# Kernel optimization log

Measured on AMD Instinct MI355X. Metric: run time of the kernel, lower is better.

Reference implementation:

```python
import jax, jax.numpy as jnp
import numpy as np

NUM_CLASSES = 7
EPS = 1e-10
BATCH = 4_000_000


def setup_inputs() -> dict:
    key = jax.random.key(0)
    k1, k2 = jax.random.split(key)
    logits = jax.random.normal(k1, (BATCH, NUM_CLASSES), dtype=jnp.float32)
    targets = jax.random.randint(k2, (BATCH,), 0, NUM_CLASSES, dtype=jnp.int32)
    return {"logits": logits, "targets": targets}


def reference(logits, targets):
    # softmax probabilities [B, C]
    probs = jax.nn.softmax(logits, axis=1)
    B = logits.shape[0]
    rows = jnp.arange(B)
    t = targets.astype(jnp.int32)
    # sum of probs at classes t-1, t, t+1, masking out-of-range neighbors
    total = probs[rows, t]
    lo = t - 1
    hi = t + 1
    total = total + jnp.where(lo >= 0, probs[rows, jnp.maximum(lo, 0)], 0.0)
    total = total + jnp.where(hi < NUM_CLASSES, probs[rows, jnp.minimum(hi, NUM_CLASSES - 1)], 0.0)
    loss = -jnp.log(total + EPS)
    return jnp.sum(loss) / B
```

## Files before the change

kernel.cpp:

```cpp
#include <hip/hip_runtime.h>
#include <hip/hip_bf16.h>

#define NUM_CLASSES 7
#define ROWS_PER_TILE 256
#define BLOCK 256
#define NBLOCKS 2048
#define F4_PER_TILE (ROWS_PER_TILE * NUM_CLASSES / 4)

__global__ __launch_bounds__(BLOCK) void pom_main(const float* __restrict__ logits,
                                                  const int* __restrict__ targets,
                                                  double* __restrict__ partials,
                                                  int B) {
    __shared__ float4 tile4[F4_PER_TILE];
    float* tile = (float*)tile4;

    const int tid = threadIdx.x;
    const int numTiles = (B + ROWS_PER_TILE - 1) / ROWS_PER_TILE;
    const float4* __restrict__ g4 = (const float4*)logits;
    const long long totalF4 = ((long long)B * NUM_CLASSES) / 4;

    float acc = 0.0f;

    for (int t = blockIdx.x; t < numTiles; t += gridDim.x) {
        const long long f4base = (long long)t * F4_PER_TILE;
        const int row = t * ROWS_PER_TILE + tid;

        int tg = 0;
        if (row < B) tg = targets[row];
        float4 a = make_float4(0.f, 0.f, 0.f, 0.f);
        float4 b = make_float4(0.f, 0.f, 0.f, 0.f);
        if (f4base + tid < totalF4)        a = g4[f4base + tid];
        if (tid < F4_PER_TILE - BLOCK && f4base + BLOCK + tid < totalF4)
                                           b = g4[f4base + BLOCK + tid];

        __syncthreads();
        tile4[tid] = a;
        if (tid < F4_PER_TILE - BLOCK) tile4[BLOCK + tid] = b;
        __syncthreads();

        if (row < B) {
            const float* l = tile + tid * NUM_CLASSES;
            float lv[7];
            #pragma unroll
            for (int i = 0; i < NUM_CLASSES; ++i) lv[i] = l[i];

            float m = lv[0];
            #pragma unroll
            for (int i = 1; i < NUM_CLASSES; ++i) m = fmaxf(m, lv[i]);

            float s = 0.0f, w = 0.0f;
            #pragma unroll
            for (int i = 0; i < NUM_CLASSES; ++i) {
                float e = __expf(lv[i] - m);
                s += e;
                bool in = (i >= tg - 1) && (i <= tg + 1);
                w += in ? e : 0.0f;
            }
            float total = w / s;
            acc += -__logf(total + 1e-10f);
        }
    }

    double d = (double)acc;
    #pragma unroll
    for (int off = 32; off > 0; off >>= 1) d += __shfl_down(d, off, 64);

    __shared__ double wsum[BLOCK / 64];
    if ((tid & 63) == 0) wsum[tid >> 6] = d;
    __syncthreads();
    if (tid == 0) {
        double blk = 0.0;
        #pragma unroll
        for (int i = 0; i < BLOCK / 64; ++i) blk += wsum[i];
        partials[blockIdx.x] = blk;
    }
}

__global__ __launch_bounds__(BLOCK) void pom_finalize(const double* __restrict__ partials,
                                                      int n, float* __restrict__ out,
                                                      double invB) {
    const int tid = threadIdx.x;
    double d = 0.0;
    for (int i = tid; i < n; i += BLOCK) d += partials[i];
    #pragma unroll
    for (int off = 32; off > 0; off >>= 1) d += __shfl_down(d, off, 64);

    __shared__ double wsum[BLOCK / 64];
    if ((tid & 63) == 0) wsum[tid >> 6] = d;
    __syncthreads();
    if (tid == 0) {
        double s = 0.0;
        #pragma unroll
        for (int i = 0; i < BLOCK / 64; ++i) s += wsum[i];
        out[0] = (float)(s * invB);
    }
}

extern "C" void kernel_launch(void* const* d_in, const int* in_sizes, int n_in,
                              void* d_out, int out_size, void* d_ws, size_t ws_size,
                              hipStream_t stream) {
    const float* logits  = (const float*)d_in[0];
    const int*   targets = (const int*)d_in[1];
    const int B = in_sizes[1];
    float* out = (float*)d_out;
    double* partials = (double*)d_ws;

    pom_main<<<NBLOCKS, BLOCK, 0, stream>>>(logits, targets, partials, B);
    pom_finalize<<<1, BLOCK, 0, stream>>>(partials, NBLOCKS, out, 1.0 / (double)B);
}
```

Measured before the change: 176.6 us.

## Replace LDS tiled staging with per-thread 4-row vectorized direct loads

Each thread now loads four consecutive rows (seven float4 logits plus one int4 of targets) directly from global memory instead of staging tiles through shared memory with two barriers per tile. This removes LDS traffic and synchronization and raises memory-level parallelism per thread. A scalar tail loop handles rows not divisible by four. The strided per-thread access pattern may reduce coalescing per load instruction and increases register use.

```diff
diff --git a/kernel.cpp b/kernel.cpp
--- a/kernel.cpp
+++ b/kernel.cpp
@@ -2,47 +2,36 @@
 #include <hip/hip_bf16.h>
 
 #define NUM_CLASSES 7
-#define ROWS_PER_TILE 256
 #define BLOCK 256
 #define NBLOCKS 2048
-#define F4_PER_TILE (ROWS_PER_TILE * NUM_CLASSES / 4)
 
 __global__ __launch_bounds__(BLOCK) void pom_main(const float* __restrict__ logits,
                                                   const int* __restrict__ targets,
                                                   double* __restrict__ partials,
                                                   int B) {
-    __shared__ float4 tile4[F4_PER_TILE];
-    float* tile = (float*)tile4;
-
-    const int tid = threadIdx.x;
-    const int numTiles = (B + ROWS_PER_TILE - 1) / ROWS_PER_TILE;
+    const int tid = blockIdx.x * BLOCK + threadIdx.x;
+    const int nth = gridDim.x * BLOCK;
+    const int nChunks = B >> 2;
     const float4* __restrict__ g4 = (const float4*)logits;
-    const long long totalF4 = ((long long)B * NUM_CLASSES) / 4;
+    const int4*   __restrict__ t4 = (const int4*)targets;
 
     float acc = 0.0f;
 
-    for (int t = blockIdx.x; t < numTiles; t += gridDim.x) {
-        const long long f4base = (long long)t * F4_PER_TILE;
-        const int row = t * ROWS_PER_TILE + tid;
+    for (int c = tid; c < nChunks; c += nth) {
+        float4 v[7];
+        const float4* p = g4 + (long long)c * 7;
+        #pragma unroll
+        for (int j = 0; j < 7; ++j) v[j] = p[j];
+        const int4 tgv = t4[c];
+        const int tgs[4] = {tgv.x, tgv.y, tgv.z, tgv.w};
+        const float* f = (const float*)v;
 
-        int tg = 0;
-        if (row < B) tg = targets[row];
-        float4 a = make_float4(0.f, 0.f, 0.f, 0.f);
-        float4 b = make_float4(0.f, 0.f, 0.f, 0.f);
-        if (f4base + tid < totalF4)        a = g4[f4base + tid];
-        if (tid < F4_PER_TILE - BLOCK && f4base + BLOCK + tid < totalF4)
-                                           b = g4[f4base + BLOCK + tid];
-
-        __syncthreads();
-        tile4[tid] = a;
-        if (tid < F4_PER_TILE - BLOCK) tile4[BLOCK + tid] = b;
-        __syncthreads();
-
-        if (row < B) {
-            const float* l = tile + tid * NUM_CLASSES;
+        #pragma unroll
+        for (int r = 0; r < 4; ++r) {
+            const int tg = tgs[r];
             float lv[7];
             #pragma unroll
-            for (int i = 0; i < NUM_CLASSES; ++i) lv[i] = l[i];
+            for (int i = 0; i < NUM_CLASSES; ++i) lv[i] = f[r * 7 + i];
 
             float m = lv[0];
             #pragma unroll
@@ -56,9 +45,29 @@
                 bool in = (i >= tg - 1) && (i <= tg + 1);
                 w += in ? e : 0.0f;
             }
-            float total = w / s;
-            acc += -__logf(total + 1e-10f);
+            acc += -__logf(w / s + 1e-10f);
         }
+    }
+
+    const int tailStart = nChunks << 2;
+    for (int row = tailStart + tid; row < B; row += nth) {
+        const float* l = logits + (long long)row * NUM_CLASSES;
+        const int tg = targets[row];
+        float lv[7];
+        #pragma unroll
+        for (int i = 0; i < NUM_CLASSES; ++i) lv[i] = l[i];
+        float m = lv[0];
+        #pragma unroll
+        for (int i = 1; i < NUM_CLASSES; ++i) m = fmaxf(m, lv[i]);
+        float s = 0.0f, w = 0.0f;
+        #pragma unroll
+        for (int i = 0; i < NUM_CLASSES; ++i) {
+            float e = __expf(lv[i] - m);
+            s += e;
+            bool in = (i >= tg - 1) && (i <= tg + 1);
+            w += in ? e : 0.0f;
+        }
+        acc += -__logf(w / s + 1e-10f);
     }
 
     double d = (double)acc;
@@ -66,9 +75,9 @@
     for (int off = 32; off > 0; off >>= 1) d += __shfl_down(d, off, 64);
 
     __shared__ double wsum[BLOCK / 64];
-    if ((tid & 63) == 0) wsum[tid >> 6] = d;
+    if ((threadIdx.x & 63) == 0) wsum[threadIdx.x >> 6] = d;
     __syncthreads();
-    if (tid == 0) {
+    if (threadIdx.x == 0) {
         double blk = 0.0;
         #pragma unroll
         for (int i = 0; i < BLOCK / 64; ++i) blk += wsum[i];
```

Result: no change. 179.3 us (+1.5%).
